# Kernel optimization log

Measured on AMD Instinct MI355X. Metric: run time of the kernel, lower is better.

Reference implementation:

```python
import math
import jax, jax.numpy as jnp
import numpy as np

DIM = 2048
NUM_HEADS = 32
NUM_KV_HEADS = 8
HEAD_DIM = DIM // NUM_HEADS
KV_REPEAT = NUM_HEADS // NUM_KV_HEADS
BSZ, SEQ = 2, 2048
THRESHOLD = 0.05


def ternarize_ste(w):
    # scale = mean(|w|), clamped; ternary in {-1,0,1}; STE: fwd value is ternary,
    # grad flows straight through to w.
    scale = jnp.maximum(jnp.abs(w).mean(), 1e-6)
    ternary = jnp.where(w > THRESHOLD * scale, 1.0,
                        jnp.where(w < -THRESHOLD * scale, -1.0, 0.0)).astype(w.dtype)
    return w + jax.lax.stop_gradient(ternary - w)


def setup_inputs() -> dict:
    key = jax.random.key(0)
    kx, kq, kk, kv, ko = jax.random.split(key, 5)
    # kaiming_uniform_(a=sqrt(5)) => U(-b, b) with b = 1/sqrt(in_features)
    bound = 1.0 / math.sqrt(DIM)
    return {
        "x": jax.random.normal(kx, (BSZ, SEQ, DIM), dtype=jnp.float32),
        "wq": jax.random.uniform(kq, (DIM, DIM), jnp.float32, -bound, bound),
        "wk": jax.random.uniform(kk, (HEAD_DIM * NUM_KV_HEADS, DIM), jnp.float32, -bound, bound),
        "wv": jax.random.uniform(kv, (HEAD_DIM * NUM_KV_HEADS, DIM), jnp.float32, -bound, bound),
        "wo": jax.random.uniform(ko, (DIM, DIM), jnp.float32, -bound, bound),
    }


def reference(x, wq, wk, wv, wo):
    bsz, seq, _ = x.shape
    # BitLinear projections with ternarized weights (F.linear: x @ W^T)
    q = x @ ternarize_ste(wq).T                      # [b, s, dim]
    k = x @ ternarize_ste(wk).T                      # [b, s, kvh*hd]
    v = x @ ternarize_ste(wv).T

    q = q.reshape(bsz, seq, NUM_HEADS, HEAD_DIM)     # [b, s, H, d]
    k = k.reshape(bsz, seq, NUM_KV_HEADS, HEAD_DIM)
    v = v.reshape(bsz, seq, NUM_KV_HEADS, HEAD_DIM)
    # repeat_interleave over the kv-head axis to match query heads
    k = jnp.repeat(k, KV_REPEAT, axis=2)             # [b, s, H, d]
    v = jnp.repeat(v, KV_REPEAT, axis=2)

    scale = 1.0 / math.sqrt(HEAD_DIM)
    att = jnp.einsum('bqhd,bkhd->bhqk', q, k) * scale  # [b, H, s, s]
    causal = jnp.tril(jnp.ones((seq, seq), dtype=bool))
    att = jnp.where(causal, att, -jnp.inf)
    probs = jax.nn.softmax(att, axis=-1)
    out = jnp.einsum('bhqk,bkhd->bqhd', probs, v).reshape(bsz, seq, DIM)
    return out @ ternarize_ste(wo).T
```

## Files before the change

### kernel.cpp

```cpp
#include <hip/hip_runtime.h>

typedef _Float16 f16;
typedef f16  f16x8 __attribute__((ext_vector_type(8)));
typedef f16  f16x4 __attribute__((ext_vector_type(4)));
typedef float f32x4 __attribute__((ext_vector_type(4)));

#define DIM_   2048
#define SEQ_   2048
#define BATCH_ 2
#define MROWS_ (BATCH_*SEQ_)
#define HD_    64
#define KVW_   512

__device__ __forceinline__ f32x4 mfma16(f16x8 a, f16x8 b, f32x4 c) {
  return __builtin_amdgcn_mfma_f32_16x16x32_f16(a, b, c, 0, 0, 0);
}

typedef const __attribute__((address_space(1))) void gas_void;
typedef __attribute__((address_space(3))) void las_void;
__device__ __forceinline__ void gload16(const void* g, void* l) {
  __builtin_amdgcn_global_load_lds((gas_void*)g, (las_void*)l, 16, 0, 0);
}

__device__ __forceinline__ unsigned long long pk4(float a, float b, float c, float d) {
  union { _Float16 h[4]; unsigned long long u; } z;
  auto p0 = __builtin_amdgcn_cvt_pkrtz(a, b);
  auto p1 = __builtin_amdgcn_cvt_pkrtz(c, d);
  z.h[0] = p0[0]; z.h[1] = p0[1]; z.h[2] = p1[0]; z.h[3] = p1[1];
  return z.u;
}

__global__ __launch_bounds__(256)
void abssum_part(const float* __restrict__ w0, const float* __restrict__ w1,
                 const float* __restrict__ w2, const float* __restrict__ w3,
                 float* __restrict__ parts) {
  const int id = blockIdx.y;
  const float* w = id == 0 ? w0 : id == 1 ? w1 : id == 2 ? w2 : w3;
  const int n4 = (id == 1 || id == 2) ? (KVW_ * DIM_ / 4) : (DIM_ * DIM_ / 4);
  float s = 0.f;
  for (int i = blockIdx.x * 256 + threadIdx.x; i < n4; i += gridDim.x * 256) {
    float4 v = *(const float4*)(w + (long)i * 4);
    s += fabsf(v.x) + fabsf(v.y) + fabsf(v.z) + fabsf(v.w);
  }
  #pragma unroll
  for (int off = 32; off > 0; off >>= 1)
    s += __shfl_down(s, off, 64);
  __shared__ float red[4];
  int lane = threadIdx.x & 63, wv = threadIdx.x >> 6;
  if (lane == 0) red[wv] = s;
  __syncthreads();
  if (threadIdx.x == 0)
    parts[id * 192 + blockIdx.x] = (red[0] + red[1]) + (red[2] + red[3]);
}

__global__ __launch_bounds__(256)
void abssum_fin(const float* __restrict__ parts, float* __restrict__ sums) {
  const int wv = threadIdx.x >> 6, lane = threadIdx.x & 63;
  float s = parts[wv * 192 + lane] + parts[wv * 192 + 64 + lane]
          + parts[wv * 192 + 128 + lane];
  #pragma unroll
  for (int off = 32; off > 0; off >>= 1)
    s += __shfl_down(s, off, 64);
  if (lane == 0) sums[wv] = s;
}

__global__ __launch_bounds__(256)
void ternarize4(const float* __restrict__ w0, const float* __restrict__ w1,
                const float* __restrict__ w2, const float* __restrict__ w3,
                unsigned short* __restrict__ t0, unsigned short* __restrict__ t1,
                unsigned short* __restrict__ t2, unsigned short* __restrict__ t3,
                const float* __restrict__ sums) {
  const int id = blockIdx.y;
  const float* w = id == 0 ? w0 : id == 1 ? w1 : id == 2 ? w2 : w3;
  unsigned short* t = id == 0 ? t0 : id == 1 ? t1 : id == 2 ? t2 : t3;
  const int n = (id == 1 || id == 2) ? (KVW_ * DIM_) : (DIM_ * DIM_);
  const float thr = 0.05f * fmaxf(sums[id] / (float)n, 1e-6f);
  const int n4 = n >> 2;
  for (int i = blockIdx.x * 256 + threadIdx.x; i < n4; i += gridDim.x * 256) {
    float4 v = *(const float4*)(w + (long)i * 4);
    ushort4 o;
    o.x = v.x > thr ? 0x3C00 : (v.x < -thr ? 0xBC00 : 0);
    o.y = v.y > thr ? 0x3C00 : (v.y < -thr ? 0xBC00 : 0);
    o.z = v.z > thr ? 0x3C00 : (v.z < -thr ? 0xBC00 : 0);
    o.w = v.w > thr ? 0x3C00 : (v.w < -thr ? 0xBC00 : 0);
    *(ushort4*)(t + (long)i * 4) = o;
  }
}

__global__ __launch_bounds__(256)
void splitx_kernel(const float* __restrict__ x, int n4,
                   f16* __restrict__ hi, f16* __restrict__ lo) {
  int stride = gridDim.x * 256;
  for (int i = blockIdx.x * 256 + threadIdx.x; i < n4; i += stride) {
    float4 v = *(const float4*)(x + (long)i * 4);
    f16x4 h, l;
    h[0] = (f16)v.x; l[0] = (f16)(v.x - (float)h[0]);
    h[1] = (f16)v.y; l[1] = (f16)(v.y - (float)h[1]);
    h[2] = (f16)v.z; l[2] = (f16)(v.z - (float)h[2]);
    h[3] = (f16)v.w; l[3] = (f16)(v.w - (float)h[3]);
    *(f16x4*)(hi + (long)i * 4) = h;
    *(f16x4*)(lo + (long)i * 4) = l;
  }
}

template<bool SPLIT, int OUTMODE>
__global__ __launch_bounds__(256)
void gemm_nt(const f16* __restrict__ Ah, const f16* __restrict__ Al,
             const f16* __restrict__ B, float* __restrict__ C,
             f16* __restrict__ O1, f16* __restrict__ O2,
             f16* __restrict__ K1, f16* __restrict__ K2,
             f16* __restrict__ OV, int M, int N, int K) {
  constexpr int BUFSZ = SPLIT ? 24576 : 16384;
  __shared__ __attribute__((aligned(16))) char smem[2 * BUFSZ];

  const int cpx = gridDim.x >> 3;
  const int id2 = (blockIdx.x & 7) * cpx + (blockIdx.x >> 3);
  const int nbx = N >> 7;
  const int bx  = id2 % nbx;
  const int by  = id2 / nbx;
  const int brow = by * 128;
  const int bcol = bx * 128;

  const int tid  = threadIdx.x;
  const int lane = tid & 63;
  const int wv   = tid >> 6;
  const int wr   = (wv >> 1) * 64;
  const int wc   = (wv & 1) * 64;
  const int fr   = lane & 15;
  const int fq   = lane >> 4;

  const bool lo_on = SPLIT && (OUTMODE != 3 || bcol < 2560);

  const int srw = wv * 32 + (lane >> 2);
  const int scg = ((lane & 3) ^ ((lane >> 3) & 3)) * 8;
  const f16* gA0 = Ah + (long)(brow + srw) * K + scg;
  const f16* gA1 = gA0 + 16 * (long)K;
  const f16* gB0 = B + (long)(bcol + srw) * K + scg;
  const f16* gB1 = gB0 + 16 * (long)K;
  const f16* gL0 = SPLIT ? (Al + (long)(brow + srw) * K + scg) : nullptr;
  const f16* gL1 = SPLIT ? (gL0 + 16 * (long)K) : nullptr;
  const int wvb = __builtin_amdgcn_readfirstlane(wv * 1024);

  auto STAGE = [&](int kt, int buf) {
    const int k0 = kt * 32;
    char* base = smem + buf * BUFSZ;
    f16* lA = (f16*)base + wvb;
    f16* lB = (f16*)(base + (SPLIT ? 16384 : 8192)) + wvb;
    gload16(gA0 + k0, lA);
    gload16(gA1 + k0, lA + 512);
    gload16(gB0 + k0, lB);
    gload16(gB1 + k0, lB + 512);
    if (lo_on) {
      f16* lL = (f16*)(base + 8192) + wvb;
      gload16(gL0 + k0, lL);
      gload16(gL1 + k0, lL + 512);
    }
  };

  const int xga = (fq ^ ((fr >> 1) & 3)) * 8;

  f32x4 acc[4][4] = {};
  const int nk = K >> 5;

  STAGE(0, 0);
  #pragma unroll 1
  for (int kt = 0; kt < nk; ++kt) {
    asm volatile("s_waitcnt vmcnt(0)" ::: "memory");
    __syncthreads();
    if (kt + 1 < nk) STAGE(kt + 1, (kt + 1) & 1);

    const char* base = smem + (kt & 1) * BUFSZ;
    const f16* cAh = (const f16*)base;
    const f16* cAl = (const f16*)(base + 8192);
    const f16* cB  = (const f16*)(base + (SPLIT ? 16384 : 8192));

    f16x8 bfr[4];
    #pragma unroll
    for (int ni = 0; ni < 4; ++ni)
      bfr[ni] = *(const f16x8*)(cB + (wc + ni * 16 + fr) * 32 + xga);
    #pragma unroll
    for (int mi = 0; mi < 4; ++mi) {
      const int aoff = (wr + mi * 16 + fr) * 32 + xga;
      f16x8 ah = *(const f16x8*)(cAh + aoff);
      #pragma unroll
      for (int ni = 0; ni < 4; ++ni)
        acc[mi][ni] = mfma16(ah, bfr[ni], acc[mi][ni]);
      if (lo_on) {
        f16x8 al = *(const f16x8*)(cAl + aoff);
        #pragma unroll
        for (int ni = 0; ni < 4; ++ni)
          acc[mi][ni] = mfma16(al, bfr[ni], acc[mi][ni]);
      }
    }
  }

  if constexpr (OUTMODE == 0) {
    #pragma unroll
    for (int mi = 0; mi < 4; ++mi)
      #pragma unroll
      for (int ni = 0; ni < 4; ++ni)
        #pragma unroll
        for (int r = 0; r < 4; ++r)
          C[(long)(brow + wr + mi * 16 + fq * 4 + r) * N + (bcol + wc + ni * 16 + fr)]
              = acc[mi][ni][r];
  } else {
    const int colbase = bcol + wc;
    if (colbase < 2048) {
      #pragma unroll
      for (int mi = 0; mi < 4; ++mi)
        #pragma unroll
        for (int ni = 0; ni < 4; ++ni)
          #pragma unroll
          for (int r = 0; r < 4; ++r) {
            long idx = (long)(brow + wr + mi * 16 + fq * 4 + r) * DIM_
                     + colbase + ni * 16 + fr;
            float v = acc[mi][ni][r];
            f16 hv = (f16)v;
            O1[idx] = hv;
            O2[idx] = (f16)(v - (float)hv);
          }
    } else if (colbase < 2560) {
      #pragma unroll
      for (int mi = 0; mi < 4; ++mi)
        #pragma unroll
        for (int ni = 0; ni < 4; ++ni)
          #pragma unroll
          for (int r = 0; r < 4; ++r) {
            long idx = (long)(brow + wr + mi * 16 + fq * 4 + r) * KVW_
                     + (colbase - 2048) + ni * 16 + fr;
            float v = acc[mi][ni][r];
            f16 hv = (f16)v;
            K1[idx] = hv;
            K2[idx] = (f16)(v - (float)hv);
          }
    } else {
      f16* sT = (f16*)smem;
      const int khh = (colbase - 2560) >> 6;
      const int bb  = brow >> 11;
      const int s0  = (brow & (SEQ_ - 1)) + wr;
      f16* st = sT + wv * 32 * 72;
      #pragma unroll
      for (int nh = 0; nh < 2; ++nh) {
        #pragma unroll
        for (int nj = 0; nj < 2; ++nj) {
          const int ni = nh * 2 + nj;
          #pragma unroll
          for (int mi = 0; mi < 4; ++mi)
            #pragma unroll
            for (int r = 0; r < 4; ++r)
              st[(nj * 16 + fr) * 72 + mi * 16 + fq * 4 + r] = (f16)acc[mi][ni][r];
        }
        #pragma unroll
        for (int i = 0; i < 4; ++i) {
          int dl = i * 8 + (lane >> 3);
          f16x8 v = *(const f16x8*)(st + dl * 72 + (lane & 7) * 8);
          *(f16x8*)(OV + ((long)(bb * 8 + khh) * 64 + nh * 32 + dl) * SEQ_
                    + s0 + (lane & 7) * 8) = v;
        }
      }
    }
  }
}

__global__ __launch_bounds__(256, 2)
void attn_kernel(const f16* __restrict__ qhi, const f16* __restrict__ qlo,
                 const f16* __restrict__ khi, const f16* __restrict__ klo,
                 const f16* __restrict__ vt,  f16* __restrict__ AO) {
  const int id2  = (blockIdx.x & 7) * 64 + (blockIdx.x >> 3);
  const int pr   = id2 & 31;
  const int cmb  = id2 >> 5;
  const int kh   = cmb & 7;
  const int b    = cmb >> 3;
  const int tid  = threadIdx.x;
  const int lane = tid & 63;
  const int w    = tid >> 6;
  const int fr   = lane & 15;
  const int fq   = lane >> 4;
  const int h    = kh * 4 + w;
  const int xr   = (fr & 7) << 4;

  __shared__ __attribute__((aligned(16))) char sKh[2][64 * 128];
  __shared__ __attribute__((aligned(16))) char sKl[2][64 * 128];
  __shared__ __attribute__((aligned(16))) char sVt[2][64 * 128];
  __shared__ __attribute__((aligned(16))) char sP [4][2][16 * 128];

  const int srow = w * 16 + (lane >> 3);
  const int scol = ((lane & 7) ^ (lane >> 3)) * 8;
  const f16* gK0 = khi + ((long)(b * SEQ_) + srow) * KVW_ + kh * HD_ + scol;
  const f16* gL0 = klo + ((long)(b * SEQ_) + srow) * KVW_ + kh * HD_ + scol;
  const f16* gV0 = vt + ((long)(b * 8 + kh) * HD_ + srow) * SEQ_ + scol;
  const int ldso = __builtin_amdgcn_readfirstlane(w * 2048);

  auto STAGE = [&](int kb, int buf) {
    const long ko = (long)kb * 64 * KVW_;
    const long vo = (long)kb * 64;
    gload16(gK0 + ko,             (char*)sKh[buf] + ldso);
    gload16(gK0 + ko + 8 * KVW_,  (char*)sKh[buf] + ldso + 1024);
    gload16(gL0 + ko,             (char*)sKl[buf] + ldso);
    gload16(gL0 + ko + 8 * KVW_,  (char*)sKl[buf] + ldso + 1024);
    gload16(gV0 + vo,             (char*)sVt[buf] + ldso);
    gload16(gV0 + vo + 8 * SEQ_,  (char*)sVt[buf] + ldso + 1024);
  };

  char* pw0 = sP[w][0];
  char* pw1 = sP[w][1];
  const float ce = 0.125f * 1.44269504f;

  #pragma unroll 1
  for (int pass = 0; pass < 2; ++pass) {
    const int t     = pass ? (63 - pr) : pr;
    const int nkv   = (t >> 1) + 1;
    const int qrow0 = t * 32;

    f16x8 qh[2][2], ql[2][2];
    #pragma unroll
    for (int st = 0; st < 2; ++st)
      #pragma unroll
      for (int ks = 0; ks < 2; ++ks) {
        const long qoff = (long)(b * SEQ_ + qrow0 + st * 16 + fr) * DIM_
                        + h * HD_ + ks * 32 + fq * 8;
        qh[st][ks] = *(const f16x8*)(qhi + qoff);
        ql[st][ks] = *(const f16x8*)(qlo + qoff);
      }

    __syncthreads();
    STAGE(0, 0);

    float m0 = -1e30f, m1 = -1e30f, l0 = 0.f, l1 = 0.f;
    f32x4 o0[4] = {}, o1[4] = {};
    int c = 0;

    #pragma unroll 1
    for (int kb = 0; kb < nkv; ++kb) {
      asm volatile("s_waitcnt vmcnt(0)" ::: "memory");
      __syncthreads();
      if (kb + 1 < nkv) STAGE(kb + 1, c ^ 1);
      const char* bK = sKh[c]; const char* bL = sKl[c]; const char* bV = sVt[c];

      f32x4 s0[4] = {}, s1[4] = {};
      #pragma unroll
      for (int ks = 0; ks < 2; ++ks)
        #pragma unroll
        for (int ni = 0; ni < 4; ++ni) {
          const int rb = (ni * 16 + fr) * 128 + ((ks * 64 + fq * 16) ^ xr);
          f16x8 ah = *(const f16x8*)(bK + rb);
          f16x8 af = *(const f16x8*)(bL + rb);
          s0[ni] = mfma16(ah, qh[0][ks], s0[ni]);
          s0[ni] = mfma16(ah, ql[0][ks], s0[ni]);
          s0[ni] = mfma16(af, qh[0][ks], s0[ni]);
          s1[ni] = mfma16(ah, qh[1][ks], s1[ni]);
          s1[ni] = mfma16(ah, ql[1][ks], s1[ni]);
          s1[ni] = mfma16(af, qh[1][ks], s1[ni]);
        }
      if (kb == nkv - 1) {
        #pragma unroll
        for (int ni = 0; ni < 4; ++ni)
          #pragma unroll
          for (int r = 0; r < 4; ++r) {
            const int kk = ni * 16 + fq * 4 + r;
            if (kk > (t & 1) * 32 + fr)      s0[ni][r] = -1e30f;
            if (kk > (t & 1) * 32 + 16 + fr) s1[ni][r] = -1e30f;
          }
      }

      #pragma unroll
      for (int st = 0; st < 2; ++st) {
        f32x4* s = st ? s1 : s0;
        float& m = st ? m1 : m0;
        float& l = st ? l1 : l0;
        f32x4* o = st ? o1 : o0;
        char* pw = st ? pw1 : pw0;

        float ma = fmaxf(fmaxf(s[0][0], s[0][1]), fmaxf(s[0][2], s[0][3]));
        float mb2 = fmaxf(fmaxf(s[1][0], s[1][1]), fmaxf(s[1][2], s[1][3]));
        float mc = fmaxf(fmaxf(s[2][0], s[2][1]), fmaxf(s[2][2], s[2][3]));
        float md = fmaxf(fmaxf(s[3][0], s[3][1]), fmaxf(s[3][2], s[3][3]));
        float mb = fmaxf(fmaxf(ma, mb2), fmaxf(mc, md));
        mb = fmaxf(mb, __shfl_xor(mb, 16, 64));
        mb = fmaxf(mb, __shfl_xor(mb, 32, 64));

        const float mo = m;
        const bool trig = mb > mo + 64.f;
        const float mn = trig ? mb : mo;
        m = mn;
        const float al = exp2f((mo - mn) * ce);
        const float tt = mn * ce;

        float rs = 0.f;
        #pragma unroll
        for (int ni = 0; ni < 4; ++ni) {
          #pragma unroll
          for (int r = 0; r < 4; ++r) {
            float pv = exp2f(fmaf(s[ni][r], ce, -tt));
            s[ni][r] = pv;
            rs += pv;
          }
          *(unsigned long long*)(pw + ((fr * 128 + ni * 32 + fq * 8) ^ xr)) =
              pk4(s[ni][0], s[ni][1], s[ni][2], s[ni][3]);
        }
        rs += __shfl_xor(rs, 16, 64);
        rs += __shfl_xor(rs, 32, 64);
        l = l * al + rs;

        if (__any(trig)) {
          #pragma unroll
          for (int r = 0; r < 4; ++r) {
            float alr = __shfl(al, ((lane >> 4) << 2) + r, 64);
            o[0][r] *= alr; o[1][r] *= alr; o[2][r] *= alr; o[3][r] *= alr;
          }
        }
      }

      #pragma unroll
      for (int ks = 0; ks < 2; ++ks) {
        const int pb = (fr * 128 + ks * 64 + fq * 16) ^ xr;
        f16x8 pa0 = *(const f16x8*)(pw0 + pb);
        f16x8 pa1 = *(const f16x8*)(pw1 + pb);
        #pragma unroll
        for (int di = 0; di < 4; ++di) {
          f16x8 vf = *(const f16x8*)(bV + (di * 16 + fr) * 128
                                     + ((ks * 64 + fq * 16) ^ xr));
          o0[di] = mfma16(pa0, vf, o0[di]);
          o1[di] = mfma16(pa1, vf, o1[di]);
        }
      }
      c ^= 1;
    }

    #pragma unroll
    for (int st = 0; st < 2; ++st) {
      const f32x4* o = st ? o1 : o0;
      const float l = st ? l1 : l0;
      float linv[4];
      #pragma unroll
      for (int r = 0; r < 4; ++r)
        linv[r] = 1.f / __shfl(l, ((lane >> 4) << 2) + r, 64);
      #pragma unroll
      for (int di = 0; di < 4; ++di)
        #pragma unroll
        for (int r = 0; r < 4; ++r)
          AO[(long)(b * SEQ_ + qrow0 + st * 16 + fq * 4 + r) * DIM_
             + h * HD_ + di * 16 + fr] = (f16)(o[di][r] * linv[r]);
    }
  }
}

extern "C" void kernel_launch(void* const* d_in, const int* in_sizes, int n_in,
                              void* d_out, int out_size, void* d_ws, size_t ws_size,
                              hipStream_t stream) {
  const float* x  = (const float*)d_in[0];
  const float* wq = (const float*)d_in[1];
  const float* wk = (const float*)d_in[2];
  const float* wv = (const float*)d_in[3];
  const float* wo = (const float*)d_in[4];
  char* ws = (char*)d_ws;

  size_t off = 0;
  float* sums  = (float*)ws;                off = 256;
  float* parts = (float*)(ws + off);        off += 4 * 192 * 4;  off = 4096;
  f16* x_hi  = (f16*)(ws + off);            off += (size_t)MROWS_ * DIM_ * 2;
  f16* x_lo  = (f16*)(ws + off);            off += (size_t)MROWS_ * DIM_ * 2;
  f16* wq_t  = (f16*)(ws + off);            off += (size_t)DIM_ * DIM_ * 2;
  f16* wkv_t = (f16*)(ws + off);            off += (size_t)1024 * DIM_ * 2;
  f16* wo_t  = (f16*)(ws + off);            off += (size_t)DIM_ * DIM_ * 2;
  f16* qhi   = (f16*)(ws + off);            off += (size_t)MROWS_ * DIM_ * 2;
  f16* qlo   = (f16*)(ws + off);            off += (size_t)MROWS_ * DIM_ * 2;
  f16* khi   = (f16*)(ws + off);            off += (size_t)MROWS_ * KVW_ * 2;
  f16* klo   = (f16*)(ws + off);            off += (size_t)MROWS_ * KVW_ * 2;
  f16* vtb   = (f16*)(ws + off);            off += (size_t)BATCH_ * 8 * 64 * SEQ_ * 2;
  f16* ao    = (f16*)(ws + off);            off += (size_t)MROWS_ * DIM_ * 2;

  abssum_part<<<dim3(192, 4), dim3(256), 0, stream>>>(wq, wk, wv, wo, parts);
  abssum_fin<<<dim3(1), dim3(256), 0, stream>>>(parts, sums);
  ternarize4<<<dim3(192, 4), dim3(256), 0, stream>>>(
      wq, wk, wv, wo,
      (unsigned short*)wq_t, (unsigned short*)wkv_t,
      (unsigned short*)(wkv_t + (size_t)KVW_ * DIM_), (unsigned short*)wo_t,
      sums);

  splitx_kernel<<<dim3(1024), dim3(256), 0, stream>>>(x, MROWS_ * DIM_ / 4, x_hi, x_lo);

  gemm_nt<true, 3><<<dim3((3072 / 128) * (MROWS_ / 128)), dim3(256), 0, stream>>>(
      x_hi, x_lo, wq_t, nullptr, qhi, qlo, khi, klo, vtb, MROWS_, 3072, DIM_);

  attn_kernel<<<dim3(32 * 8 * BATCH_), dim3(256), 0, stream>>>(
      qhi, qlo, khi, klo, vtb, ao);

  gemm_nt<false, 0><<<dim3((DIM_ / 128) * (MROWS_ / 128)), dim3(256), 0, stream>>>(
      ao, ao, wo_t, (float*)d_out, nullptr, nullptr, nullptr, nullptr, nullptr,
      MROWS_, DIM_, DIM_);
}
```

Baseline: 318.0 us.

## Triple-buffer GEMM loads and merge prep kernels to cut launches

Result: no change. 323.0 us (+1.6%).

```diff
diff --git a/kernel.cpp b/kernel.cpp
--- a/kernel.cpp
+++ b/kernel.cpp
@@ -31,37 +31,42 @@
 }
 
 __global__ __launch_bounds__(256)
-void abssum_part(const float* __restrict__ w0, const float* __restrict__ w1,
-                 const float* __restrict__ w2, const float* __restrict__ w3,
-                 float* __restrict__ parts) {
+void prep1(const float* __restrict__ x,
+           const float* __restrict__ w0, const float* __restrict__ w1,
+           const float* __restrict__ w2, const float* __restrict__ w3,
+           float* __restrict__ parts, f16* __restrict__ hi, f16* __restrict__ lo) {
   const int id = blockIdx.y;
-  const float* w = id == 0 ? w0 : id == 1 ? w1 : id == 2 ? w2 : w3;
-  const int n4 = (id == 1 || id == 2) ? (KVW_ * DIM_ / 4) : (DIM_ * DIM_ / 4);
-  float s = 0.f;
-  for (int i = blockIdx.x * 256 + threadIdx.x; i < n4; i += gridDim.x * 256) {
-    float4 v = *(const float4*)(w + (long)i * 4);
-    s += fabsf(v.x) + fabsf(v.y) + fabsf(v.z) + fabsf(v.w);
-  }
-  #pragma unroll
-  for (int off = 32; off > 0; off >>= 1)
-    s += __shfl_down(s, off, 64);
-  __shared__ float red[4];
-  int lane = threadIdx.x & 63, wv = threadIdx.x >> 6;
-  if (lane == 0) red[wv] = s;
-  __syncthreads();
-  if (threadIdx.x == 0)
-    parts[id * 192 + blockIdx.x] = (red[0] + red[1]) + (red[2] + red[3]);
-}
-
-__global__ __launch_bounds__(256)
-void abssum_fin(const float* __restrict__ parts, float* __restrict__ sums) {
-  const int wv = threadIdx.x >> 6, lane = threadIdx.x & 63;
-  float s = parts[wv * 192 + lane] + parts[wv * 192 + 64 + lane]
-          + parts[wv * 192 + 128 + lane];
-  #pragma unroll
-  for (int off = 32; off > 0; off >>= 1)
-    s += __shfl_down(s, off, 64);
-  if (lane == 0) sums[wv] = s;
+  if (id < 4) {
+    const float* w = id == 0 ? w0 : id == 1 ? w1 : id == 2 ? w2 : w3;
+    const int n4 = (id == 1 || id == 2) ? (KVW_ * DIM_ / 4) : (DIM_ * DIM_ / 4);
+    float s = 0.f;
+    for (int i = blockIdx.x * 256 + threadIdx.x; i < n4; i += gridDim.x * 256) {
+      float4 v = *(const float4*)(w + (long)i * 4);
+      s += fabsf(v.x) + fabsf(v.y) + fabsf(v.z) + fabsf(v.w);
+    }
+    #pragma unroll
+    for (int off = 32; off > 0; off >>= 1)
+      s += __shfl_down(s, off, 64);
+    __shared__ float red[4];
+    int lane = threadIdx.x & 63, wv = threadIdx.x >> 6;
+    if (lane == 0) red[wv] = s;
+    __syncthreads();
+    if (threadIdx.x == 0)
+      parts[id * 192 + blockIdx.x] = (red[0] + red[1]) + (red[2] + red[3]);
+  } else {
+    const int half = (MROWS_ * DIM_ / 4) / 2;
+    const long base = (long)(id - 4) * half;
+    for (int i = blockIdx.x * 256 + threadIdx.x; i < half; i += gridDim.x * 256) {
+      float4 v = *(const float4*)(x + (base + i) * 4);
+      f16x4 h, l;
+      h[0] = (f16)v.x; l[0] = (f16)(v.x - (float)h[0]);
+      h[1] = (f16)v.y; l[1] = (f16)(v.y - (float)h[1]);
+      h[2] = (f16)v.z; l[2] = (f16)(v.z - (float)h[2]);
+      h[3] = (f16)v.w; l[3] = (f16)(v.w - (float)h[3]);
+      *(f16x4*)(hi + (base + i) * 4) = h;
+      *(f16x4*)(lo + (base + i) * 4) = l;
+    }
+  }
 }
 
 __global__ __launch_bounds__(256)
@@ -69,12 +74,25 @@
                 const float* __restrict__ w2, const float* __restrict__ w3,
                 unsigned short* __restrict__ t0, unsigned short* __restrict__ t1,
                 unsigned short* __restrict__ t2, unsigned short* __restrict__ t3,
-                const float* __restrict__ sums) {
+                const float* __restrict__ parts) {
   const int id = blockIdx.y;
   const float* w = id == 0 ? w0 : id == 1 ? w1 : id == 2 ? w2 : w3;
   unsigned short* t = id == 0 ? t0 : id == 1 ? t1 : id == 2 ? t2 : t3;
   const int n = (id == 1 || id == 2) ? (KVW_ * DIM_) : (DIM_ * DIM_);
-  const float thr = 0.05f * fmaxf(sums[id] / (float)n, 1e-6f);
+
+  __shared__ float thr_s;
+  if (threadIdx.x < 64) {
+    const int lane = threadIdx.x;
+    float s = parts[id * 192 + lane] + parts[id * 192 + 64 + lane]
+            + parts[id * 192 + 128 + lane];
+    #pragma unroll
+    for (int off = 32; off > 0; off >>= 1)
+      s += __shfl_down(s, off, 64);
+    if (lane == 0) thr_s = 0.05f * fmaxf(s / (float)n, 1e-6f);
+  }
+  __syncthreads();
+  const float thr = thr_s;
+
   const int n4 = n >> 2;
   for (int i = blockIdx.x * 256 + threadIdx.x; i < n4; i += gridDim.x * 256) {
     float4 v = *(const float4*)(w + (long)i * 4);
@@ -87,22 +105,6 @@
   }
 }
 
-__global__ __launch_bounds__(256)
-void splitx_kernel(const float* __restrict__ x, int n4,
-                   f16* __restrict__ hi, f16* __restrict__ lo) {
-  int stride = gridDim.x * 256;
-  for (int i = blockIdx.x * 256 + threadIdx.x; i < n4; i += stride) {
-    float4 v = *(const float4*)(x + (long)i * 4);
-    f16x4 h, l;
-    h[0] = (f16)v.x; l[0] = (f16)(v.x - (float)h[0]);
-    h[1] = (f16)v.y; l[1] = (f16)(v.y - (float)h[1]);
-    h[2] = (f16)v.z; l[2] = (f16)(v.z - (float)h[2]);
-    h[3] = (f16)v.w; l[3] = (f16)(v.w - (float)h[3]);
-    *(f16x4*)(hi + (long)i * 4) = h;
-    *(f16x4*)(lo + (long)i * 4) = l;
-  }
-}
-
 template<bool SPLIT, int OUTMODE>
 __global__ __launch_bounds__(256)
 void gemm_nt(const f16* __restrict__ Ah, const f16* __restrict__ Al,
@@ -111,7 +113,7 @@
              f16* __restrict__ K1, f16* __restrict__ K2,
              f16* __restrict__ OV, int M, int N, int K) {
   constexpr int BUFSZ = SPLIT ? 24576 : 16384;
-  __shared__ __attribute__((aligned(16))) char smem[2 * BUFSZ];
+  __shared__ __attribute__((aligned(16))) char smem[3 * BUFSZ];
 
   const int cpx = gridDim.x >> 3;
   const int id2 = (blockIdx.x & 7) * cpx + (blockIdx.x >> 3);
@@ -163,13 +165,19 @@
   const int nk = K >> 5;
 
   STAGE(0, 0);
+  STAGE(1, 1);
   #pragma unroll 1
   for (int kt = 0; kt < nk; ++kt) {
-    asm volatile("s_waitcnt vmcnt(0)" ::: "memory");
-    __syncthreads();
-    if (kt + 1 < nk) STAGE(kt + 1, (kt + 1) & 1);
-
-    const char* base = smem + (kt & 1) * BUFSZ;
+    if (kt < nk - 1) {
+      if (lo_on) asm volatile("s_waitcnt vmcnt(6)" ::: "memory");
+      else       asm volatile("s_waitcnt vmcnt(4)" ::: "memory");
+    } else {
+      asm volatile("s_waitcnt vmcnt(0)" ::: "memory");
+    }
+    __builtin_amdgcn_s_barrier();
+    if (kt + 2 < nk) STAGE(kt + 2, (kt + 2) % 3);
+
+    const char* base = smem + (kt % 3) * BUFSZ;
     const f16* cAh = (const f16*)base;
     const f16* cAl = (const f16*)(base + 8192);
     const f16* cB  = (const f16*)(base + (SPLIT ? 16384 : 8192));
@@ -234,7 +242,7 @@
             K2[idx] = (f16)(v - (float)hv);
           }
     } else {
-      f16* sT = (f16*)smem;
+      f16* sT = (f16*)(smem + BUFSZ);
       const int khh = (colbase - 2560) >> 6;
       const int bb  = brow >> 11;
       const int s0  = (brow & (SEQ_ - 1)) + wr;
@@ -456,8 +464,7 @@
   char* ws = (char*)d_ws;
 
   size_t off = 0;
-  float* sums  = (float*)ws;                off = 256;
-  float* parts = (float*)(ws + off);        off += 4 * 192 * 4;  off = 4096;
+  float* parts = (float*)ws;                off = 4096;
   f16* x_hi  = (f16*)(ws + off);            off += (size_t)MROWS_ * DIM_ * 2;
   f16* x_lo  = (f16*)(ws + off);            off += (size_t)MROWS_ * DIM_ * 2;
   f16* wq_t  = (f16*)(ws + off);            off += (size_t)DIM_ * DIM_ * 2;
@@ -470,15 +477,13 @@
   f16* vtb   = (f16*)(ws + off);            off += (size_t)BATCH_ * 8 * 64 * SEQ_ * 2;
   f16* ao    = (f16*)(ws + off);            off += (size_t)MROWS_ * DIM_ * 2;
 
-  abssum_part<<<dim3(192, 4), dim3(256), 0, stream>>>(wq, wk, wv, wo, parts);
-  abssum_fin<<<dim3(1), dim3(256), 0, stream>>>(parts, sums);
+  prep1<<<dim3(192, 6), dim3(256), 0, stream>>>(x, wq, wk, wv, wo,
+                                                parts, x_hi, x_lo);
   ternarize4<<<dim3(192, 4), dim3(256), 0, stream>>>(
       wq, wk, wv, wo,
       (unsigned short*)wq_t, (unsigned short*)wkv_t,
       (unsigned short*)(wkv_t + (size_t)KVW_ * DIM_), (unsigned short*)wo_t,
-      sums);
-
-  splitx_kernel<<<dim3(1024), dim3(256), 0, stream>>>(x, MROWS_ * DIM_ / 4, x_hi, x_lo);
+      parts);
 
   gemm_nt<true, 3><<<dim3((3072 / 128) * (MROWS_ / 128)), dim3(256), 0, stream>>>(
       x_hi, x_lo, wq_t, nullptr, qhi, qlo, khi, klo, vtb, MROWS_, 3072, DIM_);
```
